# Kernel optimization log

Hardware: AMD Instinct MI355X
Metric: run time of the kernel (lower is better)

The kernel has to match this reference:

```python
import jax, jax.numpy as jnp
import numpy as np

PAD = 32       # F.pad(..., (32,32,32,32))
N_INST = 32    # labels in [0, 32]; one-hot drops background -> 32 instance channels
EPS = 1e-6


def _lovasz_hinge_flat(logits, labels):
    # logits, labels: [P] flattened over instances*H*W (per_image=False)
    signs = 2.0 * labels - 1.0
    errors = 1.0 - logits * signs
    order = jnp.argsort(-errors)               # descending sort of errors
    errors_sorted = errors[order]
    labels_sorted = labels[order]
    gts = jnp.sum(labels_sorted)
    inter = gts - jnp.cumsum(labels_sorted)
    union = gts + jnp.cumsum(1.0 - labels_sorted)
    jaccard = 1.0 - inter / union
    grad = jnp.concatenate([jaccard[:1], jaccard[1:] - jaccard[:-1]])
    return jnp.dot(jax.nn.relu(errors_sorted), jax.lax.stop_gradient(grad))


def _per_image_loss(emb, w, gt, W1, b1, W2, b2):
    # emb: [C,H,W], w: [1,H,W], gt: [1,H,W] int
    emb = jnp.pad(emb, ((0, 0), (PAD, PAD), (PAD, PAD)))
    w = jnp.pad(w, ((0, 0), (PAD, PAD), (PAD, PAD)))[0]      # [H',W']
    gt = jnp.pad(gt, ((0, 0), (PAD, PAD), (PAD, PAD)))[0]    # [H',W']
    # one-hot over instance ids 1..N_INST (background dropped): [N,H',W']
    oh = (gt[None, :, :] == jnp.arange(1, N_INST + 1)[:, None, None]).astype(emb.dtype)
    # weighted per-instance counts and centroids
    counts = jnp.einsum('nhw,hw->n', oh, w) + EPS                     # [N]
    centers = jnp.einsum('nhw,chw,hw->nc', oh, emb, w) / counts[:, None]  # [N,C]
    # sims = centers broadcast minus embeddings: [N,C,H',W']
    sims = centers[:, :, None, None] - emb[None]
    # per-pixel classifier MLP (flatten -> Linear -> ReLU -> Linear -> fold)
    h = jax.nn.relu(jnp.einsum('nchw,ck->nkhw', sims, W1) + b1[None, :, None, None])
    logits = jnp.einsum('nkhw,k->nhw', h, W2[:, 0]) + b2[0]           # probs[:,0]
    return _lovasz_hinge_flat(logits.reshape(-1), oh.reshape(-1))


def setup_inputs() -> dict:
    key = jax.random.key(0)
    k = jax.random.split(key, 8)
    B, C, H, Wd, HID = 4, 16, 192, 192, 32
    return {
        'y_embeddings': jax.random.normal(k[0], (B, C, H, Wd), jnp.float32),
        'y_weights': jax.random.uniform(k[1], (B, 1, H, Wd), jnp.float32),
        'y_true': jax.random.randint(k[2], (B, 1, H, Wd), 0, N_INST + 1),
        'W1': jax.random.normal(k[3], (C, HID), jnp.float32) * 0.1,
        'b1': jnp.zeros((HID,), jnp.float32),
        'W2': jax.random.normal(k[4], (HID, 1), jnp.float32) * 0.1,
        'b2': jnp.zeros((1,), jnp.float32),
    }


def reference(y_embeddings, y_weights, y_true, W1, b1, W2, b2):
    # random labels over 192^2 pixels guarantee every image has positives,
    # so the torch `if torch.any(gt>0)` branch is always taken -> plain mean.
    losses = jax.vmap(_per_image_loss, in_axes=(0, 0, 0, None, None, None, None))(
        y_embeddings, y_weights, y_true, W1, b1, W2, b2)
    return jnp.mean(losses)
```

## Files before the change

kernel.cpp:

```cpp
#include <hip/hip_runtime.h>

#define NBINS 4096
#define B 4
#define C 16
#define HID 32
#define NI 32
#define INTER 36864
#define PADMULT 28672
#define EPSF 1e-6f
#define THR 256
#define BPI 144
#define NBLK (B * BPI)

#define OFF_COUNTS 0
#define OFF_CSUMS  (OFF_COUNTS + B*NI)
#define OFF_V      (OFF_CSUMS + B*NI*C)
#define OFF_PERR   (OFF_V + B*NI*HID)
#define OFF_MKEY   (OFF_PERR + B*NI)
#define OFF_RANGE  (OFF_MKEY + B)
#define CTRL_END   (OFF_RANGE + 2*B)
#define OFF_HCNT   8192
#define OFF_FCNT   (OFF_HCNT + NBLK*NBINS)
#define OFF_FPOS   (OFF_FCNT + B*NBINS)

__device__ inline unsigned fmap(float f) {
    unsigned u = __float_as_uint(f);
    return (u & 0x80000000u) ? ~u : (u | 0x80000000u);
}
__device__ inline float funmap(unsigned k) {
    return (k & 0x80000000u) ? __uint_as_float(k & 0x7fffffffu)
                             : __uint_as_float(~k);
}

__global__ void k_init(unsigned* wsu, float* out) {
    int i = threadIdx.x;
    if (i < CTRL_END) wsu[i] = 0u;
    if (i == 0) out[0] = 0.f;
}

__global__ __launch_bounds__(THR, 4) void k_stats(
        const float* __restrict__ emb, const float* __restrict__ wgt,
        const int* __restrict__ gt, float* ws, unsigned* wsu) {
    __shared__ float s_cnt[NI];
    __shared__ float s_sum[NI * 17];
    __shared__ unsigned s_mk;
    int tid = threadIdx.x, bx = blockIdx.x;
    int img = bx / BPI;
    int q = (bx - img * BPI) * THR + tid;
    for (int i = tid; i < NI; i += THR) s_cnt[i] = 0.f;
    for (int i = tid; i < NI * 17; i += THR) s_sum[i] = 0.f;
    if (tid == 0) s_mk = 0u;
    __syncthreads();

    int g = gt[img * INTER + q];
    const float* ep = emb + (size_t)img * C * INTER + q;
    float e[C];
    float nrm = 0.f;
    #pragma unroll
    for (int c = 0; c < C; c++) { e[c] = ep[c * INTER]; nrm = fmaf(e[c], e[c], nrm); }
    if (g > 0) {
        float wv = wgt[img * INTER + q];
        atomicAdd(&s_cnt[g - 1], wv);
        #pragma unroll
        for (int c = 0; c < C; c++)
            atomicAdd(&s_sum[(g - 1) * 17 + c], e[c] * wv);
    }
    atomicMax(&s_mk, fmap(nrm));
    __syncthreads();
    for (int i = tid; i < NI; i += THR)
        atomicAdd(&ws[OFF_COUNTS + img * NI + i], s_cnt[i]);
    for (int i = tid; i < NI * C; i += THR) {
        int n = i / C, c = i - n * C;
        atomicAdd(&ws[OFF_CSUMS + (img * NI + n) * C + c], s_sum[n * 17 + c]);
    }
    if (tid == 0) atomicMax(&wsu[OFF_MKEY + img], s_mk);
}

__global__ void k_centers(const float* __restrict__ W1, const float* __restrict__ b1,
                          const float* __restrict__ W2, const float* __restrict__ b2,
                          float* ws, unsigned* wsu) {
    int im = blockIdx.x, tid = threadIdx.x;
    __shared__ float s_v[NI * HID];
    __shared__ float s_a[HID];
    __shared__ unsigned s_lo, s_hi;
    float b2v = b2[0];
    float M = sqrtf(funmap(wsu[OFF_MKEY + im]));
    if (tid < HID) {
        float ssq = 0.f;
        #pragma unroll
        for (int c = 0; c < C; c++)
            ssq = fmaf(W1[c * HID + tid], W1[c * HID + tid], ssq);
        s_a[tid] = M * sqrtf(ssq);
    }
    if (tid == 0) { s_lo = 0xFFFFFFFFu; s_hi = 0u; }
    for (int idx = tid; idx < NI * HID; idx += THR) {
        int n = idx >> 5, k = idx & 31;
        float cv = ws[OFF_COUNTS + im * NI + n] + EPSF;
        float acc = b1[k];
        #pragma unroll
        for (int c = 0; c < C; c++)
            acc += (ws[OFF_CSUMS + (im * NI + n) * C + c] / cv) * W1[c * HID + k];
        s_v[idx] = acc;
        ws[OFF_V + im * NI * HID + idx] = acc;
    }
    __syncthreads();
    if (tid < NI) {
        float lo = b2v, hi = b2v, lgp = b2v;
        #pragma unroll
        for (int k = 0; k < HID; k++) {
            float vk = s_v[tid * HID + k], a = s_a[k], w = W2[k];
            float thi = fmaxf(vk + a, 0.f), tlo = fmaxf(vk - a, 0.f);
            hi += w * (w > 0.f ? thi : tlo);
            lo += w * (w > 0.f ? tlo : thi);
            lgp = fmaf(fmaxf(vk, 0.f), w, lgp);
        }
        float pe = 1.f + lgp;
        ws[OFF_PERR + im * NI + tid] = pe;
        atomicMin(&s_lo, fmap(fminf(1.f - hi, 1.f + lo)));
        atomicMax(&s_hi, fmap(fmaxf(1.f - lo, 1.f + hi)));
    }
    __syncthreads();
    if (tid == 0) {
        ((float*)wsu)[OFF_RANGE + im * 2]     = funmap(s_lo);
        ((float*)wsu)[OFF_RANGE + im * 2 + 1] = funmap(s_hi);
    }
}

__global__ __launch_bounds__(THR, 4) void k_hist(
        const float* __restrict__ emb, const int* __restrict__ gt,
        const float* __restrict__ W1, const float* __restrict__ W2,
        const float* __restrict__ b2, const float* __restrict__ ws,
        unsigned* wsu) {
    __shared__ unsigned s_h[NBINS];
    int tid = threadIdx.x, bx = blockIdx.x;
    int img = bx / BPI;
    int q = (bx - img * BPI) * THR + tid;
    for (int i = tid; i < NBINS; i += THR) s_h[i] = 0u;
    float emin = ((const float*)wsu)[OFF_RANGE + img * 2];
    float emax = ((const float*)wsu)[OFF_RANGE + img * 2 + 1];
    float invbw = (float)NBINS / fmaxf(emax - emin, 1e-20f);
    float b2v = b2[0];
    const float* vimg = ws + OFF_V + img * NI * HID;
    __syncthreads();

    const float* ep = emb + (size_t)img * C * INTER + q;
    float u[HID];
    #pragma unroll
    for (int k = 0; k < HID; k++) u[k] = 0.f;
    #pragma unroll
    for (int c = 0; c < C; c++) {
        float ev = ep[c * INTER];
        #pragma unroll
        for (int k = 0; k < HID; k++) u[k] = fmaf(ev, W1[c * HID + k], u[k]);
    }
    int g = gt[img * INTER + q];
    for (int n = 0; n < NI; n++) {
        const float* vn = vimg + n * HID;
        float lg0 = b2v, lg1 = 0.f, lg2 = 0.f, lg3 = 0.f;
        #pragma unroll
        for (int k = 0; k < HID; k += 4) {
            lg0 = fmaf(fmaxf(vn[k + 0] - u[k + 0], 0.f), W2[k + 0], lg0);
            lg1 = fmaf(fmaxf(vn[k + 1] - u[k + 1], 0.f), W2[k + 1], lg1);
            lg2 = fmaf(fmaxf(vn[k + 2] - u[k + 2], 0.f), W2[k + 2], lg2);
            lg3 = fmaf(fmaxf(vn[k + 3] - u[k + 3], 0.f), W2[k + 3], lg3);
        }
        float lg = (lg0 + lg1) + (lg2 + lg3);
        bool pos = (g == n + 1);
        float err = pos ? (1.f - lg) : (1.f + lg);
        int bn = (int)((emax - err) * invbw);
        bn = bn < 0 ? 0 : (bn >= NBINS ? NBINS - 1 : bn);
        atomicAdd(&s_h[bn], pos ? 0x10001u : 1u);
    }
    __syncthreads();
    unsigned* gc = wsu + OFF_HCNT + (size_t)bx * NBINS;
    for (int i = tid; i < NBINS; i += THR) gc[i] = s_h[i];
}

__global__ void k_reduce(unsigned* wsu) {
    int tid = threadIdx.x, b = blockIdx.x;
    int img = b >> 4;
    int bn = (b & 15) * 256 + tid;
    unsigned cnt = 0, pos = 0;
    for (int r = 0; r < BPI; r++) {
        unsigned pk = wsu[OFF_HCNT + (size_t)(img * BPI + r) * NBINS + bn];
        cnt += pk & 0xFFFFu;
        pos += pk >> 16;
    }
    wsu[OFF_FCNT + img * NBINS + bn] = cnt;
    wsu[OFF_FPOS + img * NBINS + bn] = pos;
}

__global__ void k_loss(const float* ws, const unsigned* wsu, float* out) {
    const int T = 256, CHUNK = NBINS / T;
    int img = blockIdx.x, tid = threadIdx.x;
    __shared__ unsigned s_cnt[NBINS], s_pos[NBINS];
    __shared__ float s_sum[NBINS];
    __shared__ unsigned s_pc[T], s_pp[T];
    __shared__ double s_a[T];
    float emin = ((const float*)wsu)[OFF_RANGE + img * 2];
    float emax = ((const float*)wsu)[OFF_RANGE + img * 2 + 1];
    float bw = (emax - emin) / (float)NBINS;
    float invbw = (float)NBINS / fmaxf(emax - emin, 1e-20f);
    for (int i = tid; i < NBINS; i += T) {
        unsigned cv = wsu[OFF_FCNT + img * NBINS + i];
        s_cnt[i] = cv;
        s_pos[i] = wsu[OFF_FPOS + img * NBINS + i];
        float center = emax - ((float)i + 0.5f) * bw;
        s_sum[i] = (float)cv * fmaxf(center, 0.f);
    }
    __syncthreads();
    if (tid < NI) {
        float pe = ws[OFF_PERR + img * NI + tid];
        int bn = (int)((emax - pe) * invbw);
        bn = bn < 0 ? 0 : (bn >= NBINS ? NBINS - 1 : bn);
        atomicAdd(&s_cnt[bn], (unsigned)PADMULT);
        atomicAdd(&s_sum[bn], (float)PADMULT * fmaxf(pe, 0.f));
    }
    __syncthreads();
    unsigned ccnt = 0, cpos = 0;
    for (int j = 0; j < CHUNK; j++) {
        int bn = tid * CHUNK + j;
        ccnt += s_cnt[bn]; cpos += s_pos[bn];
    }
    s_pc[tid] = ccnt; s_pp[tid] = cpos;
    __syncthreads();
    for (int off = 1; off < T; off <<= 1) {
        unsigned ac = 0, ap = 0;
        if (tid >= off) { ac = s_pc[tid - off]; ap = s_pp[tid - off]; }
        __syncthreads();
        s_pc[tid] += ac; s_pp[tid] += ap;
        __syncthreads();
    }
    double Gd = (double)s_pp[T - 1];
    double r = (double)(s_pc[tid] - ccnt);
    double L = (double)(s_pp[tid] - cpos);
    double Jprev = 1.0 - (Gd - L) / (Gd + r - L);
    double acc = 0.0;
    for (int j = 0; j < CHUNK; j++) {
        int bn = tid * CHUNK + j;
        unsigned cv = s_cnt[bn], pv = s_pos[bn];
        if (cv) {
            r += (double)cv; L += (double)pv;
            double J = 1.0 - (Gd - L) / (Gd + r - L);
            double mean = (double)s_sum[bn] / (double)cv;
            acc += mean * (J - Jprev);
            Jprev = J;
        }
    }
    s_a[tid] = acc;
    __syncthreads();
    for (int s = T / 2; s > 0; s >>= 1) {
        if (tid < s) s_a[tid] += s_a[tid + s];
        __syncthreads();
    }
    if (tid == 0) atomicAdd(out, (float)(s_a[0] * 0.25));
}

extern "C" void kernel_launch(void* const* d_in, const int* in_sizes, int n_in,
                              void* d_out, int out_size, void* d_ws, size_t ws_size,
                              hipStream_t stream) {
    const float* emb = (const float*)d_in[0];
    const float* wgt = (const float*)d_in[1];
    const int*   gt  = (const int*)d_in[2];
    const float* W1  = (const float*)d_in[3];
    const float* b1  = (const float*)d_in[4];
    const float* W2  = (const float*)d_in[5];
    const float* b2  = (const float*)d_in[6];
    float* out = (float*)d_out;
    float* ws  = (float*)d_ws;
    unsigned* wsu = (unsigned*)d_ws;

    k_init<<<1, 256, 0, stream>>>(wsu, out);
    k_stats<<<NBLK, THR, 0, stream>>>(emb, wgt, gt, ws, wsu);
    k_centers<<<B, THR, 0, stream>>>(W1, b1, W2, b2, ws, wsu);
    k_hist<<<NBLK, THR, 0, stream>>>(emb, gt, W1, W2, b2, ws, wsu);
    k_reduce<<<64, 256, 0, stream>>>(wsu);
    k_loss<<<B, 256, 0, stream>>>(ws, wsu, out);
}
```

Measured before the change: 145.5 us.

## Drop init kernel via per-block partials and vectorize hist math with packed FMA

Each k_stats block now writes its counts, centroid sums and max-norm to its own slots in the workspace instead of using global atomics, and k_centers reduces those partials. That removes the zeroing kernel and the global atomic contention. k_loss becomes a single block that loops over all four images and writes the output directly rather than accumulating it atomically. k_hist uses two-wide float vector FMA/max builtins, which may map to packed FP32 instructions. The trade-offs are extra serial reduction work in k_centers and k_loss, and the packed path depends on the builtins being available.

```diff
diff --git a/kernel.cpp b/kernel.cpp
--- a/kernel.cpp
+++ b/kernel.cpp
@@ -12,16 +12,23 @@
 #define BPI 144
 #define NBLK (B * BPI)
 
-#define OFF_COUNTS 0
-#define OFF_CSUMS  (OFF_COUNTS + B*NI)
-#define OFF_V      (OFF_CSUMS + B*NI*C)
-#define OFF_PERR   (OFF_V + B*NI*HID)
-#define OFF_MKEY   (OFF_PERR + B*NI)
-#define OFF_RANGE  (OFF_MKEY + B)
-#define CTRL_END   (OFF_RANGE + 2*B)
-#define OFF_HCNT   8192
-#define OFF_FCNT   (OFF_HCNT + NBLK*NBINS)
-#define OFF_FPOS   (OFF_FCNT + B*NBINS)
+#define OFF_PCNT  0
+#define OFF_PSUM  (OFF_PCNT + NBLK*NI)
+#define OFF_PMK   (OFF_PSUM + NBLK*NI*C)
+#define OFF_V     (OFF_PMK + NBLK)
+#define OFF_PERR  (OFF_V + B*NI*HID)
+#define OFF_RANGE (OFF_PERR + B*NI)
+#define OFF_HCNT  320000
+#define OFF_FCNT  (OFF_HCNT + NBLK*NBINS)
+#define OFF_FPOS  (OFF_FCNT + B*NBINS)
+
+#if defined(__has_builtin)
+#if __has_builtin(__builtin_elementwise_fma) && __has_builtin(__builtin_elementwise_max)
+#define USE_PK 1
+#endif
+#endif
+
+typedef float v2f __attribute__((ext_vector_type(2)));
 
 __device__ inline unsigned fmap(float f) {
     unsigned u = __float_as_uint(f);
@@ -32,15 +39,9 @@
                              : __uint_as_float(~k);
 }
 
-__global__ void k_init(unsigned* wsu, float* out) {
-    int i = threadIdx.x;
-    if (i < CTRL_END) wsu[i] = 0u;
-    if (i == 0) out[0] = 0.f;
-}
-
 __global__ __launch_bounds__(THR, 4) void k_stats(
         const float* __restrict__ emb, const float* __restrict__ wgt,
-        const int* __restrict__ gt, float* ws, unsigned* wsu) {
+        const int* __restrict__ gt, float* ws) {
     __shared__ float s_cnt[NI];
     __shared__ float s_sum[NI * 17];
     __shared__ unsigned s_mk;
@@ -68,23 +69,45 @@
     atomicMax(&s_mk, fmap(nrm));
     __syncthreads();
     for (int i = tid; i < NI; i += THR)
-        atomicAdd(&ws[OFF_COUNTS + img * NI + i], s_cnt[i]);
+        ws[OFF_PCNT + bx * NI + i] = s_cnt[i];
     for (int i = tid; i < NI * C; i += THR) {
         int n = i / C, c = i - n * C;
-        atomicAdd(&ws[OFF_CSUMS + (img * NI + n) * C + c], s_sum[n * 17 + c]);
-    }
-    if (tid == 0) atomicMax(&wsu[OFF_MKEY + img], s_mk);
+        ws[OFF_PSUM + bx * (NI * C) + i] = s_sum[n * 17 + c];
+    }
+    if (tid == 0) ws[OFF_PMK + bx] = funmap(s_mk);
 }
 
 __global__ void k_centers(const float* __restrict__ W1, const float* __restrict__ b1,
                           const float* __restrict__ W2, const float* __restrict__ b2,
                           float* ws, unsigned* wsu) {
     int im = blockIdx.x, tid = threadIdx.x;
+    __shared__ float s_cnt[NI];
+    __shared__ float s_cs[NI * C];
+    __shared__ float s_mx[THR];
     __shared__ float s_v[NI * HID];
     __shared__ float s_a[HID];
     __shared__ unsigned s_lo, s_hi;
-    float b2v = b2[0];
-    float M = sqrtf(funmap(wsu[OFF_MKEY + im]));
+
+    for (int idx = tid; idx < NI * C; idx += THR) {
+        float s = 0.f;
+        for (int r = 0; r < BPI; r++)
+            s += ws[OFF_PSUM + (size_t)(im * BPI + r) * (NI * C) + idx];
+        s_cs[idx] = s;
+    }
+    if (tid < NI) {
+        float s = 0.f;
+        for (int r = 0; r < BPI; r++)
+            s += ws[OFF_PCNT + (im * BPI + r) * NI + tid];
+        s_cnt[tid] = s;
+    }
+    s_mx[tid] = (tid < BPI) ? ws[OFF_PMK + im * BPI + tid] : 0.f;
+    if (tid == 0) { s_lo = 0xFFFFFFFFu; s_hi = 0u; }
+    __syncthreads();
+    for (int s = THR / 2; s > 0; s >>= 1) {
+        if (tid < s) s_mx[tid] = fmaxf(s_mx[tid], s_mx[tid + s]);
+        __syncthreads();
+    }
+    float M = sqrtf(s_mx[0]);
     if (tid < HID) {
         float ssq = 0.f;
         #pragma unroll
@@ -92,18 +115,18 @@
             ssq = fmaf(W1[c * HID + tid], W1[c * HID + tid], ssq);
         s_a[tid] = M * sqrtf(ssq);
     }
-    if (tid == 0) { s_lo = 0xFFFFFFFFu; s_hi = 0u; }
     for (int idx = tid; idx < NI * HID; idx += THR) {
         int n = idx >> 5, k = idx & 31;
-        float cv = ws[OFF_COUNTS + im * NI + n] + EPSF;
+        float cv = s_cnt[n] + EPSF;
         float acc = b1[k];
         #pragma unroll
         for (int c = 0; c < C; c++)
-            acc += (ws[OFF_CSUMS + (im * NI + n) * C + c] / cv) * W1[c * HID + k];
+            acc += (s_cs[n * C + c] / cv) * W1[c * HID + k];
         s_v[idx] = acc;
         ws[OFF_V + im * NI * HID + idx] = acc;
     }
     __syncthreads();
+    float b2v = b2[0];
     if (tid < NI) {
         float lo = b2v, hi = b2v, lgp = b2v;
         #pragma unroll
@@ -144,16 +167,50 @@
     __syncthreads();
 
     const float* ep = emb + (size_t)img * C * INTER + q;
-    float u[HID];
-    #pragma unroll
-    for (int k = 0; k < HID; k++) u[k] = 0.f;
+    int g = gt[img * INTER + q];
+#ifdef USE_PK
+    const v2f* W12 = (const v2f*)W1;
+    const v2f* W22 = (const v2f*)W2;
+    const v2f z2 = {0.f, 0.f};
+    v2f u2[HID / 2];
+    #pragma unroll
+    for (int j = 0; j < HID / 2; j++) u2[j] = z2;
     #pragma unroll
     for (int c = 0; c < C; c++) {
         float ev = ep[c * INTER];
+        v2f ev2 = {ev, ev};
+        #pragma unroll
+        for (int j = 0; j < HID / 2; j++)
+            u2[j] = __builtin_elementwise_fma(ev2, W12[c * (HID / 2) + j], u2[j]);
+    }
+    for (int n = 0; n < NI; n++) {
+        const v2f* vn2 = (const v2f*)(vimg + n * HID);
+        v2f a0 = z2, a1 = z2;
+        #pragma unroll
+        for (int j = 0; j < HID / 2; j += 2) {
+            a0 = __builtin_elementwise_fma(
+                     __builtin_elementwise_max(vn2[j] - u2[j], z2), W22[j], a0);
+            a1 = __builtin_elementwise_fma(
+                     __builtin_elementwise_max(vn2[j + 1] - u2[j + 1], z2), W22[j + 1], a1);
+        }
+        v2f a = a0 + a1;
+        float lg = b2v + a.x + a.y;
+        bool pos = (g == n + 1);
+        float err = pos ? (1.f - lg) : (1.f + lg);
+        int bn = (int)((emax - err) * invbw);
+        bn = bn < 0 ? 0 : (bn >= NBINS ? NBINS - 1 : bn);
+        atomicAdd(&s_h[bn], pos ? 0x10001u : 1u);
+    }
+#else
+    float u[HID];
+    #pragma unroll
+    for (int k = 0; k < HID; k++) u[k] = 0.f;
+    #pragma unroll
+    for (int c = 0; c < C; c++) {
+        float ev = ep[c * INTER];
         #pragma unroll
         for (int k = 0; k < HID; k++) u[k] = fmaf(ev, W1[c * HID + k], u[k]);
     }
-    int g = gt[img * INTER + q];
     for (int n = 0; n < NI; n++) {
         const float* vn = vimg + n * HID;
         float lg0 = b2v, lg1 = 0.f, lg2 = 0.f, lg3 = 0.f;
@@ -171,6 +228,7 @@
         bn = bn < 0 ? 0 : (bn >= NBINS ? NBINS - 1 : bn);
         atomicAdd(&s_h[bn], pos ? 0x10001u : 1u);
     }
+#endif
     __syncthreads();
     unsigned* gc = wsu + OFF_HCNT + (size_t)bx * NBINS;
     for (int i = tid; i < NBINS; i += THR) gc[i] = s_h[i];
@@ -192,68 +250,75 @@
 
 __global__ void k_loss(const float* ws, const unsigned* wsu, float* out) {
     const int T = 256, CHUNK = NBINS / T;
-    int img = blockIdx.x, tid = threadIdx.x;
+    int tid = threadIdx.x;
     __shared__ unsigned s_cnt[NBINS], s_pos[NBINS];
     __shared__ float s_sum[NBINS];
     __shared__ unsigned s_pc[T], s_pp[T];
     __shared__ double s_a[T];
-    float emin = ((const float*)wsu)[OFF_RANGE + img * 2];
-    float emax = ((const float*)wsu)[OFF_RANGE + img * 2 + 1];
-    float bw = (emax - emin) / (float)NBINS;
-    float invbw = (float)NBINS / fmaxf(emax - emin, 1e-20f);
-    for (int i = tid; i < NBINS; i += T) {
-        unsigned cv = wsu[OFF_FCNT + img * NBINS + i];
-        s_cnt[i] = cv;
-        s_pos[i] = wsu[OFF_FPOS + img * NBINS + i];
-        float center = emax - ((float)i + 0.5f) * bw;
-        s_sum[i] = (float)cv * fmaxf(center, 0.f);
-    }
-    __syncthreads();
-    if (tid < NI) {
-        float pe = ws[OFF_PERR + img * NI + tid];
-        int bn = (int)((emax - pe) * invbw);
-        bn = bn < 0 ? 0 : (bn >= NBINS ? NBINS - 1 : bn);
-        atomicAdd(&s_cnt[bn], (unsigned)PADMULT);
-        atomicAdd(&s_sum[bn], (float)PADMULT * fmaxf(pe, 0.f));
-    }
-    __syncthreads();
-    unsigned ccnt = 0, cpos = 0;
-    for (int j = 0; j < CHUNK; j++) {
-        int bn = tid * CHUNK + j;
-        ccnt += s_cnt[bn]; cpos += s_pos[bn];
-    }
-    s_pc[tid] = ccnt; s_pp[tid] = cpos;
-    __syncthreads();
-    for (int off = 1; off < T; off <<= 1) {
-        unsigned ac = 0, ap = 0;
-        if (tid >= off) { ac = s_pc[tid - off]; ap = s_pp[tid - off]; }
-        __syncthreads();
-        s_pc[tid] += ac; s_pp[tid] += ap;
-        __syncthreads();
-    }
-    double Gd = (double)s_pp[T - 1];
-    double r = (double)(s_pc[tid] - ccnt);
-    double L = (double)(s_pp[tid] - cpos);
-    double Jprev = 1.0 - (Gd - L) / (Gd + r - L);
-    double acc = 0.0;
-    for (int j = 0; j < CHUNK; j++) {
-        int bn = tid * CHUNK + j;
-        unsigned cv = s_cnt[bn], pv = s_pos[bn];
-        if (cv) {
-            r += (double)cv; L += (double)pv;
-            double J = 1.0 - (Gd - L) / (Gd + r - L);
-            double mean = (double)s_sum[bn] / (double)cv;
-            acc += mean * (J - Jprev);
-            Jprev = J;
-        }
-    }
-    s_a[tid] = acc;
-    __syncthreads();
-    for (int s = T / 2; s > 0; s >>= 1) {
-        if (tid < s) s_a[tid] += s_a[tid + s];
-        __syncthreads();
-    }
-    if (tid == 0) atomicAdd(out, (float)(s_a[0] * 0.25));
+    __shared__ double s_tot;
+    if (tid == 0) s_tot = 0.0;
+
+    for (int img = 0; img < B; ++img) {
+        float emin = ((const float*)wsu)[OFF_RANGE + img * 2];
+        float emax = ((const float*)wsu)[OFF_RANGE + img * 2 + 1];
+        float bw = (emax - emin) / (float)NBINS;
+        float invbw = (float)NBINS / fmaxf(emax - emin, 1e-20f);
+        for (int i = tid; i < NBINS; i += T) {
+            unsigned cv = wsu[OFF_FCNT + img * NBINS + i];
+            s_cnt[i] = cv;
+            s_pos[i] = wsu[OFF_FPOS + img * NBINS + i];
+            float center = emax - ((float)i + 0.5f) * bw;
+            s_sum[i] = (float)cv * fmaxf(center, 0.f);
+        }
+        __syncthreads();
+        if (tid < NI) {
+            float pe = ws[OFF_PERR + img * NI + tid];
+            int bn = (int)((emax - pe) * invbw);
+            bn = bn < 0 ? 0 : (bn >= NBINS ? NBINS - 1 : bn);
+            atomicAdd(&s_cnt[bn], (unsigned)PADMULT);
+            atomicAdd(&s_sum[bn], (float)PADMULT * fmaxf(pe, 0.f));
+        }
+        __syncthreads();
+        unsigned ccnt = 0, cpos = 0;
+        for (int j = 0; j < CHUNK; j++) {
+            int bn = tid * CHUNK + j;
+            ccnt += s_cnt[bn]; cpos += s_pos[bn];
+        }
+        s_pc[tid] = ccnt; s_pp[tid] = cpos;
+        __syncthreads();
+        for (int off = 1; off < T; off <<= 1) {
+            unsigned ac = 0, ap = 0;
+            if (tid >= off) { ac = s_pc[tid - off]; ap = s_pp[tid - off]; }
+            __syncthreads();
+            s_pc[tid] += ac; s_pp[tid] += ap;
+            __syncthreads();
+        }
+        double Gd = (double)s_pp[T - 1];
+        double r = (double)(s_pc[tid] - ccnt);
+        double L = (double)(s_pp[tid] - cpos);
+        double Jprev = 1.0 - (Gd - L) / (Gd + r - L);
+        double acc = 0.0;
+        for (int j = 0; j < CHUNK; j++) {
+            int bn = tid * CHUNK + j;
+            unsigned cv = s_cnt[bn], pv = s_pos[bn];
+            if (cv) {
+                r += (double)cv; L += (double)pv;
+                double J = 1.0 - (Gd - L) / (Gd + r - L);
+                double mean = (double)s_sum[bn] / (double)cv;
+                acc += mean * (J - Jprev);
+                Jprev = J;
+            }
+        }
+        s_a[tid] = acc;
+        __syncthreads();
+        for (int s = T / 2; s > 0; s >>= 1) {
+            if (tid < s) s_a[tid] += s_a[tid + s];
+            __syncthreads();
+        }
+        if (tid == 0) s_tot += s_a[0];
+        __syncthreads();
+    }
+    if (tid == 0) out[0] = (float)(s_tot * 0.25);
 }
 
 extern "C" void kernel_launch(void* const* d_in, const int* in_sizes, int n_in,
@@ -270,10 +335,9 @@
     float* ws  = (float*)d_ws;
     unsigned* wsu = (unsigned*)d_ws;
 
-    k_init<<<1, 256, 0, stream>>>(wsu, out);
-    k_stats<<<NBLK, THR, 0, stream>>>(emb, wgt, gt, ws, wsu);
+    k_stats<<<NBLK, THR, 0, stream>>>(emb, wgt, gt, ws);
     k_centers<<<B, THR, 0, stream>>>(W1, b1, W2, b2, ws, wsu);
     k_hist<<<NBLK, THR, 0, stream>>>(emb, gt, W1, W2, b2, ws, wsu);
     k_reduce<<<64, 256, 0, stream>>>(wsu);
-    k_loss<<<B, 256, 0, stream>>>(ws, wsu, out);
-}
+    k_loss<<<1, 256, 0, stream>>>(ws, wsu, out);
+}
```

Result: slower. 175.8 us (+20.9%).
